# Kernel optimization log

Measured on AMD Instinct MI355X. Metric: run time of the kernel, lower is better.

The kernel has to match this reference:

```python
import jax, jax.numpy as jnp
import numpy as np

L_LAYERS, D, H, FF_MUL = 4, 512, 8, 4
VOCAB, SEQ, MEM, CMEM, RATIO = 32000, 1024, 1024, 256, 4
DH = D // H


def _ln(x, g, b):
    mu = jnp.mean(x, -1, keepdims=True)
    var = jnp.mean((x - mu) ** 2, -1, keepdims=True)
    return (x - mu) / jnp.sqrt(var + 1e-5) * g + b


def _heads(x):
    b, n, _ = x.shape
    return x.reshape(b, n, H, -1).transpose(0, 2, 1, 3)  # [b,h,n,dh]


def _shift(x):
    # relative-position shift trick, x: [b,h,i,j] -> [b,h,i,j]
    b, h, i, j = x.shape
    x = jnp.concatenate([x, jnp.zeros((b, h, i, i), x.dtype)], -1)
    l = i + j - 1
    x = x.reshape(b, h, i * (i + j))
    pad = (-x.shape[-1]) % l
    x = jnp.pad(x, ((0, 0), (0, 0), (0, pad))).reshape(b, h, -1, l)
    return x[:, :, :i, i - 1:]


def _conv(x, w, b):
    # x: [B,L,D], w: [D_out, D_in, RATIO] (OIH), stride=RATIO
    y = jax.lax.conv_general_dilated(x.transpose(0, 2, 1), w, (RATIO,), 'VALID',
                                     dimension_numbers=('NCH', 'OIH', 'NCH'))
    return y.transpose(0, 2, 1) + b


def _full_attn(q, k, v):
    dots = jnp.einsum('bhid,bhjd->bhij', q, k) * (q.shape[-1] ** -0.5)
    return jnp.einsum('bhij,bhjd->bhid', jax.nn.softmax(dots, -1), v)


def setup_inputs() -> dict:
    key = jax.random.key(0)
    ks = jax.random.split(key, 24)
    s = 0.02
    return {
        'seq': jax.random.randint(ks[0], (4, SEQ), 0, VOCAB),
        'mask': jnp.ones((4, SEQ), dtype=bool),
        'mems': jax.random.normal(ks[1], (L_LAYERS, 4, MEM, D)) * s,
        'cmems': jax.random.normal(ks[2], (L_LAYERS, 4, CMEM, D)) * s,
        'pos_emb': jax.random.normal(ks[3], (H, CMEM + MEM + SEQ, DH)) * s,
        'embed': jax.random.normal(ks[4], (VOCAB, D)) * s,
        'ln1_g': jnp.ones((L_LAYERS, D)), 'ln1_b': jnp.zeros((L_LAYERS, D)),
        'Wq': jax.random.normal(ks[5], (L_LAYERS, D, D)) * s,
        'Wkv': jax.random.normal(ks[6], (L_LAYERS, D, 2 * D)) * s,
        'Wo': jax.random.normal(ks[7], (L_LAYERS, D, D)) * s,
        'bo': jnp.zeros((L_LAYERS, D)),
        'conv_w': jax.random.normal(ks[8], (L_LAYERS, D, D, RATIO)) * s,
        'conv_b': jnp.zeros((L_LAYERS, D)),
        'ln2_g': jnp.ones((L_LAYERS, D)), 'ln2_b': jnp.zeros((L_LAYERS, D)),
        'W1': jax.random.normal(ks[9], (L_LAYERS, D, FF_MUL * D)) * s,
        'b1': jnp.zeros((L_LAYERS, FF_MUL * D)),
        'W2': jax.random.normal(ks[10], (L_LAYERS, FF_MUL * D, D)) * s,
        'b2': jnp.zeros((L_LAYERS, D)),
    }


def _forward(seq, mask, mems, cmems, pos_emb, embed, ln1_g, ln1_b, Wq, Wkv, Wo, bo,
             conv_w, conv_b, ln2_g, ln2_b, W1, b1, W2, b2):
    scale = DH ** -0.5
    x = embed[seq]  # [b,t,d]
    maskb = mask.astype(bool)
    new_mems, new_cmems = [], []
    aux_total = jnp.zeros((), x.dtype)
    w_acc = 0.0
    for l in range(L_LAYERS):
        mem, cmem = mems[l], cmems[l]
        xn = _ln(x, ln1_g[l], ln1_b[l])
        q = _heads(xn @ Wq[l])
        kv_in = jnp.concatenate([cmem, mem, xn], 1)  # [b,kv_len,d]
        kv_len = kv_in.shape[1]
        k, v = jnp.split(kv_in @ Wkv[l], 2, -1)
        k, v = _heads(k), _heads(v)
        dots = jnp.einsum('bhid,bhjd->bhij', q, k) * scale
        pe = pos_emb[:, -kv_len:]
        dots = dots + _shift(jnp.einsum('bhid,hjd->bhij', q, pe) * scale)
        m2 = maskb[:, None, :, None] & maskb[:, None, None, :]  # [b,1,t,t]
        m2 = jnp.pad(m2, ((0, 0), (0, 0), (0, 0), (kv_len - SEQ, 0)), constant_values=True)
        dots = jnp.where(m2, dots, -jnp.finfo(dots.dtype).max)
        attn = jax.nn.softmax(dots, -1)
        w_acc = w_acc + jnp.mean(jax.lax.stop_gradient(attn), axis=(0, 1))
        out = jnp.einsum('bhij,bhjd->bhid', attn, v)
        out = out.transpose(0, 2, 1, 3).reshape(x.shape[0], SEQ, D)
        x = x + out @ Wo[l] + bo[l]
        # FIFO memory update (queue normed x, evict oldest)
        queue = jnp.concatenate([mem, xn], 1)
        old_mem, new_mem = queue[:, :-MEM], queue[:, -MEM:]
        pad_amt = old_mem.shape[1] % RATIO
        if pad_amt:
            old_mem = jnp.pad(old_mem, ((0, 0), (pad_amt, 0), (0, 0)))
        comp = _conv(old_mem, conv_w[l], conv_b[l])
        new_cmem = jnp.concatenate([cmem, comp], 1)[:, -CMEM:]
        new_mems.append(new_mem)
        new_cmems.append(new_cmem)
        # reconstruction (attention-reconstruction) aux loss
        old_mem_d = jax.lax.stop_gradient(old_mem)
        comp2 = _conv(old_mem_d, conv_w[l], conv_b[l])
        ck, cv = jnp.split(comp2 @ jax.lax.stop_gradient(Wkv[l]), 2, -1)
        ck, cv = _heads(ck), _heads(cv)
        start = kv_len - min(mem.shape[1], MEM) - SEQ
        ok = jax.lax.stop_gradient(k[:, :, start:kv_len - SEQ])
        ov = jax.lax.stop_gradient(v[:, :, start:kv_len - SEQ])
        qd = jax.lax.stop_gradient(q)
        aux_total = aux_total + jnp.mean((_full_attn(qd, ok, ov) - _full_attn(qd, ck, cv)) ** 2)
        # feed-forward block (PreNorm + Residual), exact GELU like torch nn.GELU
        xn2 = _ln(x, ln2_g[l], ln2_b[l])
        x = x + jax.nn.gelu(xn2 @ W1[l] + b1[l], approximate=False) @ W2[l] + b2[l]
    return (x, jnp.stack(new_mems), jnp.stack(new_cmems),
            aux_total / L_LAYERS, w_acc / L_LAYERS)


def reference(seq, mask, mems, cmems, pos_emb, embed, ln1_g, ln1_b, Wq, Wkv, Wo, bo,
              conv_w, conv_b, ln2_g, ln2_b, W1, b1, W2, b2):
    return _forward(seq, mask, mems, cmems, pos_emb, embed, ln1_g, ln1_b, Wq, Wkv, Wo, bo,
                    conv_w, conv_b, ln2_g, ln2_b, W1, b1, W2, b2)
```

## Files before the change

### kernel.cpp

```cpp
#include <hip/hip_runtime.h>
#include <hip/hip_bf16.h>


typedef __hip_bfloat16 bf16;
typedef short s16x8 __attribute__((ext_vector_type(8)));
typedef float f32x4 __attribute__((ext_vector_type(4)));

__device__ __forceinline__ f32x4 mfma16(s16x8 a, s16x8 b, f32x4 c) {
  return __builtin_amdgcn_mfma_f32_16x16x32_bf16(a, b, c, 0, 0, 0);
}

typedef __attribute__((address_space(1))) const void gvoid;
typedef __attribute__((address_space(3))) void lvoid;
__device__ __forceinline__ void gll16(const void* g, void* l) {
  __builtin_amdgcn_global_load_lds((gvoid*)g, (lvoid*)l, 16, 0, 0);
}

__device__ __forceinline__ float b2f(unsigned short u) {
  return __uint_as_float(((unsigned)u) << 16);
}
__device__ __forceinline__ unsigned short f2bb(float f) {
  bf16 h = __float2bfloat16(f);
  return *reinterpret_cast<unsigned short*>(&h);
}
__device__ __forceinline__ float ldf(const float* p) { return *p; }
__device__ __forceinline__ float ldf(const bf16* p) { return __bfloat162float(*p); }
__device__ __forceinline__ float4 ld4(const float* p) { return *(const float4*)p; }
__device__ __forceinline__ float4 ld4(const bf16* p) {
  const ushort4 u = *(const ushort4*)p;
  return make_float4(b2f(u.x), b2f(u.y), b2f(u.z), b2f(u.w));
}
__device__ __forceinline__ void st4(float* p, float4 r) { *(float4*)p = r; }
__device__ __forceinline__ void st4(bf16* p, float4 r) {
  *(ushort4*)p = make_ushort4(f2bb(r.x), f2bb(r.y), f2bb(r.z), f2bb(r.w));
}
__device__ __forceinline__ void stf(float* p, float v) { *p = v; }
__device__ __forceinline__ void stf(bf16* p, float v) { *p = __float2bfloat16(v); }

__global__ void probe_k(const void* ln1g, unsigned* flag) {
  if (threadIdx.x == 0) {
    const unsigned short u = *(const unsigned short*)ln1g;
    *flag = (u == 0x3F80u) ? 1u : 0u;
  }
}

template <int BM, int AMODE, bool ADD, bool BIAS, bool GELU, typename TC>
__global__ __launch_bounds__(256) void mgemm_k(
    const bf16* __restrict__ A, const int lda, const bf16* __restrict__ Bt,
    TC* __restrict__ C, const int ldc, const float* __restrict__ bias,
    const int K) {
  constexpr int NF = (BM == 128) ? 4 : 2;
  __shared__ bf16 As[BM * 64];
  __shared__ bf16 Bs[128 * 64];
  const int t = threadIdx.x, w = t >> 6, lane = t & 63;
  const int g = lane >> 4, li = lane & 15;
  const int m0 = blockIdx.y * BM, n0 = blockIdx.x << 7;
  const int wrow = (BM == 128) ? ((w >> 1) << 6) : 0;
  const int wcol = (BM == 128) ? ((w & 1) << 6) : (w << 5);
  f32x4 acc[4][NF];
#pragma unroll
  for (int mf = 0; mf < 4; mf++)
#pragma unroll
    for (int nf = 0; nf < NF; nf++)
#pragma unroll
      for (int e = 0; e < 4; e++) acc[mf][nf][e] = 0.f;
  constexpr int ACH = BM / 32;
  const int srow = lane >> 3, s8 = lane & 7;
  for (int k0 = 0; k0 < K; k0 += 64) {
    __syncthreads();
#pragma unroll
    for (int it = 0; it < ACH; it++) {
      const int chunk = w * ACH + it;
      const int row = (chunk << 3) + srow;
      const int k8 = s8 ^ (row & 7);
      const bf16* src;
      if constexpr (AMODE == 0) {
        src = A + (size_t)(m0 + row) * lda + k0 + (k8 << 3);
      } else if constexpr (AMODE == 1) {
        const int m = m0 + row;
        src = A + ((size_t)((m >> 8) * 2304 + 256) << 9) + (m & 255) * 2048 +
              k0 + (k8 << 3);
      } else {
        const int m = m0 + row;
        src = A + ((size_t)((m >> 10) * 2304 + 1280 + (m & 1023)) << 9) + k0 +
              (k8 << 3);
      }
      gll16(src, As + (chunk << 9));
    }
#pragma unroll
    for (int it = 0; it < 4; it++) {
      const int chunk = (w << 2) + it;
      const int row = (chunk << 3) + srow;
      const int k8 = s8 ^ (row & 7);
      gll16(Bt + (size_t)(n0 + row) * K + k0 + (k8 << 3), Bs + (chunk << 9));
    }
    __syncthreads();
#pragma unroll
    for (int ks = 0; ks < 2; ks++) {
      s16x8 af[4];
#pragma unroll
      for (int mf = 0; mf < 4; mf++) {
        const int row = wrow + (mf << 4) + li;
        af[mf] = *reinterpret_cast<const s16x8*>(
            As + (row << 6) + ((((ks << 2) + g) ^ (row & 7)) << 3));
      }
#pragma unroll
      for (int nf = 0; nf < NF; nf++) {
        const int col = wcol + (nf << 4) + li;
        const s16x8 bfr = *reinterpret_cast<const s16x8*>(
            Bs + (col << 6) + ((((ks << 2) + g) ^ (col & 7)) << 3));
#pragma unroll
        for (int mf = 0; mf < 4; mf++)
          acc[mf][nf] = mfma16(af[mf], bfr, acc[mf][nf]);
      }
    }
  }
#pragma unroll
  for (int mf = 0; mf < 4; mf++)
#pragma unroll
    for (int nf = 0; nf < NF; nf++) {
      const int n = n0 + wcol + (nf << 4) + li;
      const float bv = BIAS ? bias[n] : 0.f;
#pragma unroll
      for (int r = 0; r < 4; r++) {
        const int m = m0 + wrow + (mf << 4) + (g << 2) + r;
        float v = acc[mf][nf][r] + bv;
        if constexpr (GELU) v = 0.5f * v * (1.0f + erff(v * 0.70710678118f));
        TC* cp = C + (size_t)m * ldc + n;
        if constexpr (ADD)
          *cp += v;
        else
          stf(cp, v);
      }
    }
}

template <bool REL, bool DIFF, typename TO>
__global__ __launch_bounds__(256) void flash_k(
    const bf16* __restrict__ q, const bf16* __restrict__ kbase,
    const bf16* __restrict__ vbase, const int kvlen, const int ldkv,
    const int bstride, const bf16* __restrict__ pe, float2* __restrict__ ml,
    TO* __restrict__ outp, const float* __restrict__ prior,
    float* __restrict__ auxsum) {
  __shared__ short k_s[4096];
  __shared__ short v_s[4096];
  __shared__ short p_s[4096];
  __shared__ short pe_s[REL ? 8192 : 8];
  __shared__ float t_s[REL ? 5376 : 4];
  __shared__ float red_s[4];
  const int t = threadIdx.x, w = t >> 6, lane = t & 63;
  const int g = lane >> 4, li = lane & 15;
  const int i0 = blockIdx.x << 6, h = blockIdx.y, b = blockIdx.z;
  const bf16* qp =
      q + (size_t)(b * 1024 + i0 + (w << 4) + li) * 512 + (h << 6) + (g << 3);
  const s16x8 qf0 = *reinterpret_cast<const s16x8*>(qp);
  const s16x8 qf1 = *reinterpret_cast<const s16x8*>(qp + 32);
  const bf16* kpb = kbase + (size_t)b * bstride + (h << 6);
  const bf16* vpb = vbase + (size_t)b * bstride + (h << 6);
  const bf16* peh = REL ? pe + (size_t)h * 147456 : nullptr;
  float mreg[4] = {-1e30f, -1e30f, -1e30f, -1e30f};
  float lreg[4] = {0.f, 0.f, 0.f, 0.f};
  f32x4 o[4];
#pragma unroll
  for (int nt = 0; nt < 4; nt++)
#pragma unroll
    for (int e = 0; e < 4; e++) o[nt][e] = 0.f;

  for (int j0 = 0; j0 < kvlen; j0 += 64) {
    const int ub0 = j0 - i0 + 960;
    const bool doT = REL && (ub0 < 2304);
    __syncthreads();
    {
      const int r2 = t >> 3, c8 = t & 7;
#pragma unroll
      for (int it = 0; it < 2; it++) {
        const int row = (it << 5) + r2;
        const size_t gof = (size_t)(j0 + row) * ldkv + (c8 << 3);
        const s16x8 kk = *reinterpret_cast<const s16x8*>(kpb + gof);
        *reinterpret_cast<s16x8*>(
            k_s + (((row << 6) + (c8 << 3)) ^ ((row & 7) << 3))) = kk;
        const s16x8 vv = *reinterpret_cast<const s16x8*>(vpb + gof);
#pragma unroll
        for (int e = 0; e < 8; e++) {
          const int d = (c8 << 3) + e;
          v_s[((d << 6) + row) ^ (((c8 ^ e) & 7) << 3)] = vv[e];
        }
      }
      if (doT) {
#pragma unroll
        for (int it = 0; it < 4; it++) {
          const int idx = (it << 8) + t;
          const int row = idx >> 3, pc8 = idx & 7;
          const int u = ub0 + row;
          s16x8 pv = {0, 0, 0, 0, 0, 0, 0, 0};
          if (u < 2304)
            pv = *reinterpret_cast<const s16x8*>(peh + ((size_t)u << 6) + (pc8 << 3));
          *reinterpret_cast<s16x8*>(
              pe_s + (((row << 6) + (pc8 << 3)) ^ ((row & 7) << 3))) = pv;
        }
      }
    }
    __syncthreads();
    f32x4 s[4];
#pragma unroll
    for (int nt = 0; nt < 4; nt++) {
#pragma unroll
      for (int e = 0; e < 4; e++) s[nt][e] = 0.f;
      const int rb = (((nt << 4) + li) << 6) + (g << 3);
      const int sw = (li & 7) << 3;
      const s16x8 kb0 = *reinterpret_cast<const s16x8*>(k_s + (rb ^ sw));
      const s16x8 kb1 = *reinterpret_cast<const s16x8*>(k_s + ((rb + 32) ^ sw));
      s[nt] = mfma16(qf0, kb0, s[nt]);
      s[nt] = mfma16(qf1, kb1, s[nt]);
    }
    if (doT) {
      float* tw = t_s + w * 1344;
      const int urb = 48 - (w << 4);
#pragma unroll
      for (int ut = 0; ut < 5; ut++) {
        f32x4 tt;
#pragma unroll
        for (int e = 0; e < 4; e++) tt[e] = 0.f;
        const int prb = ((urb + (ut << 4) + li) << 6) + (g << 3);
        const int sw = (li & 7) << 3;
        const s16x8 pb0 = *reinterpret_cast<const s16x8*>(pe_s + (prb ^ sw));
        const s16x8 pb1 = *reinterpret_cast<const s16x8*>(pe_s + ((prb + 32) ^ sw));
        tt = mfma16(qf0, pb0, tt);
        tt = mfma16(qf1, pb1, tt);
#pragma unroll
        for (int r = 0; r < 4; r++) tw[((g << 2) + r) * 84 + (ut << 4) + li] = tt[r];
      }
#pragma unroll
      for (int nt = 0; nt < 4; nt++)
#pragma unroll
        for (int r = 0; r < 4; r++)
          s[nt][r] += tw[((g << 2) + r) * 83 + (nt << 4) + li + 15];
    }
#pragma unroll
    for (int nt = 0; nt < 4; nt++)
#pragma unroll
      for (int e = 0; e < 4; e++) s[nt][e] *= 0.125f;
    float pr[4][4];
#pragma unroll
    for (int r = 0; r < 4; r++) {
      float tm = fmaxf(fmaxf(s[0][r], s[1][r]), fmaxf(s[2][r], s[3][r]));
#pragma unroll
      for (int off = 1; off < 16; off <<= 1) tm = fmaxf(tm, __shfl_xor(tm, off));
      const float mn = fmaxf(mreg[r], tm);
      const float al = __expf(mreg[r] - mn);
      mreg[r] = mn;
      float te = 0.f;
#pragma unroll
      for (int nt = 0; nt < 4; nt++) {
        pr[nt][r] = __expf(s[nt][r] - mn);
        te += pr[nt][r];
      }
#pragma unroll
      for (int off = 1; off < 16; off <<= 1) te += __shfl_xor(te, off);
      lreg[r] = lreg[r] * al + te;
#pragma unroll
      for (int nt = 0; nt < 4; nt++) o[nt][r] *= al;
    }
    short* pw = p_s + (w << 10);
#pragma unroll
    for (int nt = 0; nt < 4; nt++)
#pragma unroll
      for (int r = 0; r < 4; r++) {
        const int il = (g << 2) + r;
        pw[((il << 6) + (nt << 4) + li) ^ ((il & 7) << 3)] = (short)f2bb(pr[nt][r]);
      }
#pragma unroll
    for (int ks = 0; ks < 2; ks++) {
      const s16x8 pa = *reinterpret_cast<const s16x8*>(
          pw + (((li << 6) + (ks << 5) + (g << 3)) ^ ((li & 7) << 3)));
#pragma unroll
      for (int nt = 0; nt < 4; nt++) {
        const int d = (nt << 4) + li;
        const s16x8 vb = *reinterpret_cast<const s16x8*>(
            v_s + (((d << 6) + (ks << 5) + (g << 3)) ^ ((((d >> 3) ^ (d & 7)) & 7) << 3)));
        o[nt] = mfma16(pa, vb, o[nt]);
      }
    }
  }
  float rl[4];
#pragma unroll
  for (int r = 0; r < 4; r++) rl[r] = 1.0f / lreg[r];
  if constexpr (REL) {
    if (li == 0) {
#pragma unroll
      for (int r = 0; r < 4; r++)
        ml[(size_t)((b << 3) + h) * 1024 + i0 + (w << 4) + (g << 2) + r] =
            make_float2(mreg[r], lreg[r]);
    }
  }
  if constexpr (!DIFF) {
#pragma unroll
    for (int nt = 0; nt < 4; nt++)
#pragma unroll
      for (int r = 0; r < 4; r++) {
        const size_t adr = (size_t)(b * 1024 + i0 + (w << 4) + (g << 2) + r) * 512 +
                           (h << 6) + (nt << 4) + li;
        stf(outp + adr, o[nt][r] * rl[r]);
      }
  } else {
    float sq = 0.f;
#pragma unroll
    for (int nt = 0; nt < 4; nt++)
#pragma unroll
      for (int r = 0; r < 4; r++) {
        const size_t adr = (size_t)(b * 1024 + i0 + (w << 4) + (g << 2) + r) * 512 +
                           (h << 6) + (nt << 4) + li;
        const float dv = o[nt][r] * rl[r] - prior[adr];
        sq = fmaf(dv, dv, sq);
      }
#pragma unroll
    for (int off = 1; off < 64; off <<= 1) sq += __shfl_xor(sq, off);
    if (lane == 0) red_s[w] = sq;
    __syncthreads();
    if (t == 0) atomicAdd(auxsum, red_s[0] + red_s[1] + red_s[2] + red_s[3]);
  }
}

__global__ __launch_bounds__(256) void wacc_k(const bf16* __restrict__ q,
                                              const bf16* __restrict__ kv,
                                              const bf16* __restrict__ pe,
                                              const float2* __restrict__ ml,
                                              float* __restrict__ w_acc) {
  __shared__ short k_s[4096];
  __shared__ short pe_s[8192];
  __shared__ float t_s[5376];
  __shared__ float2 ml_s[64];
  const int t = threadIdx.x, w = t >> 6, lane = t & 63;
  const int g = lane >> 4, li = lane & 15;
  const int i0 = blockIdx.x << 6, j0 = blockIdx.y << 6;
  const int ub0 = j0 - i0 + 960;
  const bool doT = (ub0 < 2304);
  f32x4 acc[4];
#pragma unroll
  for (int nt = 0; nt < 4; nt++)
#pragma unroll
    for (int e = 0; e < 4; e++) acc[nt][e] = 0.f;
  for (int h = 0; h < 8; h++) {
    __syncthreads();
    if (doT) {
      const bf16* peh = pe + (size_t)h * 147456;
#pragma unroll
      for (int it = 0; it < 4; it++) {
        const int idx = (it << 8) + t;
        const int row = idx >> 3, pc8 = idx & 7;
        const int u = ub0 + row;
        s16x8 pv = {0, 0, 0, 0, 0, 0, 0, 0};
        if (u < 2304)
          pv = *reinterpret_cast<const s16x8*>(peh + ((size_t)u << 6) + (pc8 << 3));
        *reinterpret_cast<s16x8*>(
            pe_s + (((row << 6) + (pc8 << 3)) ^ ((row & 7) << 3))) = pv;
      }
    }
    for (int b = 0; b < 4; b++) {
      __syncthreads();
      {
        const int r2 = t >> 3, c8 = t & 7;
        const bf16* kpb = kv + (size_t)b * 2359296 + (h << 6);
#pragma unroll
        for (int it = 0; it < 2; it++) {
          const int row = (it << 5) + r2;
          const s16x8 kk = *reinterpret_cast<const s16x8*>(
              kpb + (size_t)(j0 + row) * 1024 + (c8 << 3));
          *reinterpret_cast<s16x8*>(
              k_s + (((row << 6) + (c8 << 3)) ^ ((row & 7) << 3))) = kk;
        }
        if (t < 64) {
          float2 v = ml[(size_t)((b << 3) + h) * 1024 + i0 + t];
          v.y = 1.0f / v.y;
          ml_s[t] = v;
        }
      }
      __syncthreads();
      const bf16* qp =
          q + (size_t)(b * 1024 + i0 + (w << 4) + li) * 512 + (h << 6) + (g << 3);
      const s16x8 qf0 = *reinterpret_cast<const s16x8*>(qp);
      const s16x8 qf1 = *reinterpret_cast<const s16x8*>(qp + 32);
      f32x4 s[4];
#pragma unroll
      for (int nt = 0; nt < 4; nt++) {
#pragma unroll
        for (int e = 0; e < 4; e++) s[nt][e] = 0.f;
        const int rb = (((nt << 4) + li) << 6) + (g << 3);
        const int sw = (li & 7) << 3;
        const s16x8 kb0 = *reinterpret_cast<const s16x8*>(k_s + (rb ^ sw));
        const s16x8 kb1 = *reinterpret_cast<const s16x8*>(k_s + ((rb + 32) ^ sw));
        s[nt] = mfma16(qf0, kb0, s[nt]);
        s[nt] = mfma16(qf1, kb1, s[nt]);
      }
      if (doT) {
        float* tw = t_s + w * 1344;
        const int urb = 48 - (w << 4);
#pragma unroll
        for (int ut = 0; ut < 5; ut++) {
          f32x4 tt;
#pragma unroll
          for (int e = 0; e < 4; e++) tt[e] = 0.f;
          const int prb = ((urb + (ut << 4) + li) << 6) + (g << 3);
          const int sw = (li & 7) << 3;
          const s16x8 pb0 = *reinterpret_cast<const s16x8*>(pe_s + (prb ^ sw));
          const s16x8 pb1 = *reinterpret_cast<const s16x8*>(pe_s + ((prb + 32) ^ sw));
          tt = mfma16(qf0, pb0, tt);
          tt = mfma16(qf1, pb1, tt);
#pragma unroll
          for (int r = 0; r < 4; r++)
            tw[((g << 2) + r) * 84 + (ut << 4) + li] = tt[r];
        }
#pragma unroll
        for (int nt = 0; nt < 4; nt++)
#pragma unroll
          for (int r = 0; r < 4; r++)
            s[nt][r] += tw[((g << 2) + r) * 83 + (nt << 4) + li + 15];
      }
#pragma unroll
      for (int nt = 0; nt < 4; nt++)
#pragma unroll
        for (int r = 0; r < 4; r++) {
          const float sv = s[nt][r] * 0.125f;
          const float2 st = ml_s[(w << 4) + (g << 2) + r];
          acc[nt][r] += __expf(sv - st.x) * st.y;
        }
    }
  }
#pragma unroll
  for (int nt = 0; nt < 4; nt++)
#pragma unroll
    for (int r = 0; r < 4; r++) {
      float* wp = w_acc + (size_t)(i0 + (w << 4) + (g << 2) + r) * 2304 + j0 +
                  (nt << 4) + li;
      *wp += acc[nt][r];
    }
}

template <typename TIN>
__global__ __launch_bounds__(256) void wtr_k(
    const TIN* __restrict__ Wq, const TIN* __restrict__ Wkv,
    const TIN* __restrict__ Wo, const TIN* __restrict__ W1,
    const TIN* __restrict__ W2, bf16* __restrict__ WT,
    const unsigned* flag, unsigned want) {
  if (*flag != want) return;
  __shared__ bf16 tile[64][65];
  int bx = blockIdx.x;
  const TIN* W;
  bf16* dst;
  int N, K;
  if (bx < 64) {
    W = Wq; dst = WT; N = 512; K = 512;
  } else if (bx < 192) {
    W = Wkv; dst = WT + 262144; N = 1024; K = 512; bx -= 64;
  } else if (bx < 256) {
    W = Wo; dst = WT + 786432; N = 512; K = 512; bx -= 192;
  } else if (bx < 512) {
    W = W1; dst = WT + 1048576; N = 2048; K = 512; bx -= 256;
  } else {
    W = W2; dst = WT + 2097152; N = 512; K = 2048; bx -= 512;
  }
  const int tn = N >> 6;
  const int kt = bx / tn, nt = bx - kt * tn;
  const int k0 = kt << 6, n0 = nt << 6;
  const int t = threadIdx.x;
#pragma unroll
  for (int i = 0; i < 16; i++) {
    const int idx = (i << 8) + t;
    const int kr = idx >> 6, nc = idx & 63;
    tile[kr][nc] = __float2bfloat16(ldf(W + (size_t)(k0 + kr) * N + n0 + nc));
  }
  __syncthreads();
#pragma unroll
  for (int i = 0; i < 16; i++) {
    const int idx = (i << 8) + t;
    const int nr = idx >> 6, kc = idx & 63;
    dst[(size_t)(n0 + nr) * K + k0 + kc] = tile[kc][nr];
  }
}

template <typename TIN>
__global__ void wcp_k(const TIN* __restrict__ cw, bf16* __restrict__ WcT,
                      const unsigned* flag, unsigned want) {
  if (*flag != want) return;
  const int id = blockIdx.x * 256 + threadIdx.x;
  const int o = id >> 11, p = id & 2047;
  const int r = p >> 9, i = p & 511;
  WcT[id] = __float2bfloat16(ldf(cw + ((size_t)o << 11) + (i << 2) + r));
}

template <typename TIN>
__global__ void kvb_k(const TIN* __restrict__ cmem, const TIN* __restrict__ mem,
                      bf16* __restrict__ kvin, const unsigned* flag, unsigned want) {
  if (*flag != want) return;
  const int id = blockIdx.x * 256 + threadIdx.x;
  const int row = id >> 7, c4 = (id & 127) << 2;
  const int b = row / 1280, j = row - b * 1280;
  const TIN* src = (j < 256) ? cmem + (((size_t)(b * 256 + j)) << 9) + c4
                             : mem + (((size_t)(b * 1024 + j - 256)) << 9) + c4;
  st4(kvin + (((size_t)(b * 2304 + j)) << 9) + c4, ld4(src));
}

template <typename TIN>
__global__ void bcvt_k(const TIN* __restrict__ bo, const TIN* __restrict__ cb,
                       const TIN* __restrict__ b1, const TIN* __restrict__ b2,
                       float* __restrict__ bws, const unsigned* flag, unsigned want) {
  if (*flag != want) return;
  const int id = blockIdx.x * 256 + threadIdx.x;
  const int l = id / 3584, r = id - l * 3584;
  float v;
  if (r < 512) v = ldf(bo + l * 512 + r);
  else if (r < 1024) v = ldf(cb + l * 512 + r - 512);
  else if (r < 3072) v = ldf(b1 + l * 2048 + r - 1024);
  else v = ldf(b2 + l * 512 + r - 3072);
  bws[id] = v;
}

template <typename TIN, typename TY>
__global__ __launch_bounds__(256) void ln_k(const float* __restrict__ x,
                                            const TIN* __restrict__ g,
                                            const TIN* __restrict__ bta,
                                            TY* __restrict__ y, bf16* kvx,
                                            const unsigned* flag, unsigned want) {
  if (*flag != want) return;
  const int w = threadIdx.x >> 6, lane = threadIdx.x & 63;
  const size_t row = (size_t)blockIdx.x * 4 + w;
  const float* xr = x + row * 512;
  float v[8], s = 0, ss = 0;
#pragma unroll
  for (int i = 0; i < 8; i++) {
    v[i] = xr[lane + (i << 6)];
    s += v[i];
    ss = fmaf(v[i], v[i], ss);
  }
#pragma unroll
  for (int off = 1; off < 64; off <<= 1) {
    s += __shfl_xor(s, off);
    ss += __shfl_xor(ss, off);
  }
  const float mu = s * (1.0f / 512.0f);
  const float var = ss * (1.0f / 512.0f) - mu * mu;
  const float inv = rsqrtf(var + 1e-5f);
  bf16* k2 = kvx ? kvx + (((row >> 10) * 2304 + 1280 + (row & 1023)) << 9) : nullptr;
#pragma unroll
  for (int i = 0; i < 8; i++) {
    const int c = lane + (i << 6);
    const float val = (v[i] - mu) * inv * ldf(g + c) + ldf(bta + c);
    stf(y + row * 512 + c, val);
    if (k2) k2[c] = __float2bfloat16(val);
  }
}

template <typename TIN>
__global__ void embed_k(const int* __restrict__ seq, const TIN* __restrict__ emb,
                        float* __restrict__ x, const unsigned* flag, unsigned want) {
  if (*flag != want) return;
  const int row = blockIdx.x;
  const int tok = seq[row];
  const TIN* e = emb + (size_t)tok * 512;
  float* xr = x + (size_t)row * 512;
  for (int c = threadIdx.x; c < 512; c += 256) xr[c] = ldf(e + c);
}

template <typename TIN>
__global__ void cvtpe_k(const TIN* __restrict__ pe, bf16* __restrict__ peb,
                        const unsigned* flag, unsigned want) {
  if (*flag != want) return;
  const int i = blockIdx.x * 256 + threadIdx.x;
  peb[i] = __float2bfloat16(ldf(pe + i));
}

__global__ void zero_k(float* __restrict__ p, int n) {
  for (int i = blockIdx.x * 256 + threadIdx.x; i < n; i += gridDim.x * 256) p[i] = 0.0f;
}

template <typename TOUT>
__global__ void cpy_k(const bf16* __restrict__ s, TOUT* __restrict__ d, int n,
                      const unsigned* flag, unsigned want) {
  if (*flag != want) return;
  for (int i = blockIdx.x * 256 + threadIdx.x; i < n; i += gridDim.x * 256)
    stf(d + i, ldf(s + i));
}

template <typename TOUT>
__global__ void f2bs_k(const float* __restrict__ s, TOUT* __restrict__ d, float sc,
                       int n, const unsigned* flag, unsigned want) {
  if (*flag != want) return;
  for (int i = blockIdx.x * 256 + threadIdx.x; i < n; i += gridDim.x * 256)
    stf(d + i, s[i] * sc);
}

template <typename TOUT>
__global__ void fin_aux_k(const float* __restrict__ acc, TOUT* __restrict__ d,
                          const unsigned* flag, unsigned want) {
  if (*flag != want) return;
  if (threadIdx.x == 0) stf(d, acc[0] * (1.0f / 8388608.0f));
}

extern "C" void kernel_launch(void* const* d_in, const int* in_sizes, int n_in,
                              void* d_out, int out_size, void* d_ws, size_t ws_size,
                              hipStream_t stream) {
  typedef const bf16 CB;
  typedef const float CF;
  const int* seq = (const int*)d_in[0];
  CB *mems_b = (CB*)d_in[2], *cmems_b = (CB*)d_in[3], *pe_b = (CB*)d_in[4],
     *emb_b = (CB*)d_in[5], *l1g_b = (CB*)d_in[6], *l1b_b = (CB*)d_in[7],
     *Wq_b = (CB*)d_in[8], *Wkv_b = (CB*)d_in[9], *Wo_b = (CB*)d_in[10],
     *bo_b = (CB*)d_in[11], *cw_b = (CB*)d_in[12], *cb_b = (CB*)d_in[13],
     *l2g_b = (CB*)d_in[14], *l2b_b = (CB*)d_in[15], *W1_b = (CB*)d_in[16],
     *b1_b = (CB*)d_in[17], *W2_b = (CB*)d_in[18], *b2_b = (CB*)d_in[19];
  CF *mems_f = (CF*)d_in[2], *cmems_f = (CF*)d_in[3], *pe_f = (CF*)d_in[4],
     *emb_f = (CF*)d_in[5], *l1g_f = (CF*)d_in[6], *l1b_f = (CF*)d_in[7],
     *Wq_f = (CF*)d_in[8], *Wkv_f = (CF*)d_in[9], *Wo_f = (CF*)d_in[10],
     *bo_f = (CF*)d_in[11], *cw_f = (CF*)d_in[12], *cb_f = (CF*)d_in[13],
     *l2g_f = (CF*)d_in[14], *l2b_f = (CF*)d_in[15], *W1_f = (CF*)d_in[16],
     *b1_f = (CF*)d_in[17], *W2_f = (CF*)d_in[18], *b2_f = (CF*)d_in[19];
  bf16* outb = (bf16*)d_out;
  float* outf = (float*)d_out;

  float* ws = (float*)d_ws;
  float* x = ws;
  bf16* q = (bf16*)(ws + 2097152);
  bf16* kv = (bf16*)(ws + 3145728);
  bf16* mid = (bf16*)(ws + 3145728);
  float* region = ws + 7864320;
  bf16* attn_o = (bf16*)region;
  float* aux1 = region;
  bf16* xn2 = (bf16*)region;
  bf16* ckcv = (bf16*)(ws + 9961472);
  float* w_acc = ws + 10485760;
  bf16* cmp_ws = (bf16*)(ws + 12845056);
  float2* ml = (float2*)(ws + 13369344);
  float* auxsum = ws + 13434880;
  unsigned* flag = (unsigned*)(ws + 13434881);
  bf16* pe_w = (bf16*)(ws + 13434884);
  float* bias_ws = ws + 14024708;
  bf16* kvin = (bf16*)(ws + 14039044);
  bf16* WT = (bf16*)(ws + 16398340);

  probe_k<<<1, 64, 0, stream>>>(d_in[6], flag);
  zero_k<<<2048, 256, 0, stream>>>(w_acc, 2359296);
  zero_k<<<1, 256, 0, stream>>>(auxsum, 1);
  embed_k<bf16><<<4096, 256, 0, stream>>>(seq, emb_b, x, flag, 1);
  embed_k<float><<<4096, 256, 0, stream>>>(seq, emb_f, x, flag, 0);
  cvtpe_k<bf16><<<4608, 256, 0, stream>>>(pe_b, pe_w, flag, 1);
  cvtpe_k<float><<<4608, 256, 0, stream>>>(pe_f, pe_w, flag, 0);
  bcvt_k<bf16><<<56, 256, 0, stream>>>(bo_b, cb_b, b1_b, b2_b, bias_ws, flag, 1);
  bcvt_k<float><<<56, 256, 0, stream>>>(bo_f, cb_f, b1_f, b2_f, bias_ws, flag, 0);

  for (int l = 0; l < 4; l++) {
    bf16* xnl_b = outb + 2097152 + (size_t)l * 2097152;
    float* xnl_f = outf + 2097152 + (size_t)l * 2097152;
    bf16* cmp_b = outb + 10485760 + (size_t)l * 524288;
    float* cmp_f = outf + 10485760 + (size_t)l * 524288;
    const float* bl = bias_ws + l * 3584;

    wtr_k<bf16><<<768, 256, 0, stream>>>(Wq_b + (size_t)l * 262144,
        Wkv_b + (size_t)l * 524288, Wo_b + (size_t)l * 262144,
        W1_b + (size_t)l * 1048576, W2_b + (size_t)l * 1048576, WT, flag, 1);
    wtr_k<float><<<768, 256, 0, stream>>>(Wq_f + (size_t)l * 262144,
        Wkv_f + (size_t)l * 524288, Wo_f + (size_t)l * 262144,
        W1_f + (size_t)l * 1048576, W2_f + (size_t)l * 1048576, WT, flag, 0);
    wcp_k<bf16><<<4096, 256, 0, stream>>>(cw_b + (size_t)l * 1048576, WT + 3145728, flag, 1);
    wcp_k<float><<<4096, 256, 0, stream>>>(cw_f + (size_t)l * 1048576, WT + 3145728, flag, 0);
    kvb_k<bf16><<<2560, 256, 0, stream>>>(cmems_b + (size_t)l * 524288,
                                          mems_b + (size_t)l * 2097152, kvin, flag, 1);
    kvb_k<float><<<2560, 256, 0, stream>>>(cmems_f + (size_t)l * 524288,
                                           mems_f + (size_t)l * 2097152, kvin, flag, 0);
    ln_k<bf16, bf16><<<1024, 256, 0, stream>>>(x, l1g_b + l * 512, l1b_b + l * 512,
                                               xnl_b, kvin, flag, 1);
    ln_k<float, float><<<1024, 256, 0, stream>>>(x, l1g_f + l * 512, l1b_f + l * 512,
                                                 xnl_f, kvin, flag, 0);
    mgemm_k<64, 2, false, false, false, bf16><<<dim3(4, 64), 256, 0, stream>>>(
        kvin, 512, WT, q, 512, nullptr, 512);
    mgemm_k<128, 0, false, false, false, bf16><<<dim3(8, 72), 256, 0, stream>>>(
        kvin, 512, WT + 262144, kv, 1024, nullptr, 512);
    flash_k<true, false, bf16><<<dim3(16, 8, 4), 256, 0, stream>>>(
        q, kv, kv + 512, 2304, 1024, 2359296, pe_w, ml, attn_o, nullptr, nullptr);
    wacc_k<<<dim3(16, 36), 256, 0, stream>>>(q, kv, pe_w, ml, w_acc);
    mgemm_k<64, 0, true, true, false, float><<<dim3(4, 64), 256, 0, stream>>>(
        attn_o, 512, WT + 786432, x, 512, bl, 512);
    mgemm_k<64, 1, false, true, false, bf16><<<dim3(4, 16), 256, 0, stream>>>(
        kvin, 0, WT + 3145728, cmp_ws, 512, bl + 512, 2048);
    cpy_k<bf16><<<512, 256, 0, stream>>>(cmp_ws, cmp_b, 524288, flag, 1);
    cpy_k<float><<<512, 256, 0, stream>>>(cmp_ws, cmp_f, 524288, flag, 0);
    mgemm_k<64, 0, false, false, false, bf16><<<dim3(8, 16), 256, 0, stream>>>(
        cmp_ws, 512, WT + 262144, ckcv, 1024, nullptr, 512);
    flash_k<false, false, float><<<dim3(16, 8, 4), 256, 0, stream>>>(
        q, kv + 262144, kv + 262144 + 512, 1024, 1024, 2359296, nullptr, nullptr,
        aux1, nullptr, nullptr);
    flash_k<false, true, float><<<dim3(16, 8, 4), 256, 0, stream>>>(
        q, ckcv, ckcv + 512, 256, 1024, 262144, nullptr, nullptr,
        (float*)nullptr, aux1, auxsum);
    ln_k<bf16, bf16><<<1024, 256, 0, stream>>>(x, l2g_b + l * 512, l2b_b + l * 512,
                                               xn2, nullptr, flag, 1);
    ln_k<float, bf16><<<1024, 256, 0, stream>>>(x, l2g_f + l * 512, l2b_f + l * 512,
                                                xn2, nullptr, flag, 0);
    mgemm_k<128, 0, false, true, true, bf16><<<dim3(16, 32), 256, 0, stream>>>(
        xn2, 512, WT + 1048576, mid, 2048, bl + 1024, 512);
    mgemm_k<64, 0, true, true, false, float><<<dim3(4, 64), 256, 0, stream>>>(
        mid, 2048, WT + 2097152, x, 512, bl + 3072, 2048);
  }

  f2bs_k<bf16><<<2048, 256, 0, stream>>>(x, outb, 1.0f, 2097152, flag, 1);
  f2bs_k<float><<<2048, 256, 0, stream>>>(x, outf, 1.0f, 2097152, flag, 0);
  f2bs_k<bf16><<<2048, 256, 0, stream>>>(w_acc, outb + 12582913, 1.0f / 128.0f, 2359296, flag, 1);
  f2bs_k<float><<<2048, 256, 0, stream>>>(w_acc, outf + 12582913, 1.0f / 128.0f, 2359296, flag, 0);
  fin_aux_k<bf16><<<1, 64, 0, stream>>>(auxsum, outb + 12582912, flag, 1);
  fin_aux_k<float><<<1, 64, 0, stream>>>(auxsum, outf + 12582912, flag, 0);
}
```

Measured before the change: 2.031 ms.

## Double-buffer K/V staging in flash and wacc kernels, drop LDS pos-emb tiles

The flash and wacc attention kernels now double-buffer K tiles in LDS, staged with asynchronous global_load_lds, and prefetch the next V tile into registers, so loads overlap compute and each iteration needs one barrier instead of two. The relative-position term is computed from pos-emb fragments loaded straight into registers and shifted with cross-lane shuffles rather than LDS staging plus a float scratch buffer, which cuts LDS use and raises possible occupancy. Out-of-range pos-emb rows read from a new zero row buffer. The flash grid is flattened so the 8 heads of one query tile are adjacent, aux1 moves to its own workspace region, and wacc loops over head and batch with prefetching, at the cost of more register pressure.

```diff
diff --git a/kernel.cpp b/kernel.cpp
--- a/kernel.cpp
+++ b/kernel.cpp
@@ -139,18 +139,20 @@
 __global__ __launch_bounds__(256) void flash_k(
     const bf16* __restrict__ q, const bf16* __restrict__ kbase,
     const bf16* __restrict__ vbase, const int kvlen, const int ldkv,
-    const int bstride, const bf16* __restrict__ pe, float2* __restrict__ ml,
+    const int bstride, const bf16* __restrict__ pe,
+    const bf16* __restrict__ zrow, float2* __restrict__ ml,
     TO* __restrict__ outp, const float* __restrict__ prior,
     float* __restrict__ auxsum) {
-  __shared__ short k_s[4096];
-  __shared__ short v_s[4096];
+  __shared__ short k_s[2][4096];
+  __shared__ short v_s[2][4096];
   __shared__ short p_s[4096];
-  __shared__ short pe_s[REL ? 8192 : 8];
-  __shared__ float t_s[REL ? 5376 : 4];
-  __shared__ float red_s[4];
   const int t = threadIdx.x, w = t >> 6, lane = t & 63;
   const int g = lane >> 4, li = lane & 15;
-  const int i0 = blockIdx.x << 6, h = blockIdx.y, b = blockIdx.z;
+  const int bid = blockIdx.x;
+  const int h = bid & 7;
+  const int sl = bid >> 3;
+  const int b = sl >> 4;
+  const int i0 = (sl & 15) << 6;
   const bf16* qp =
       q + (size_t)(b * 1024 + i0 + (w << 4) + li) * 512 + (h << 6) + (g << 3);
   const s16x8 qf0 = *reinterpret_cast<const s16x8*>(qp);
@@ -158,6 +160,8 @@
   const bf16* kpb = kbase + (size_t)b * bstride + (h << 6);
   const bf16* vpb = vbase + (size_t)b * bstride + (h << 6);
   const bf16* peh = REL ? pe + (size_t)h * 147456 : nullptr;
+  const int vr = t >> 3, vc8 = t & 7;
+  const int kr = lane >> 3, kc8 = lane & 7;
   float mreg[4] = {-1e30f, -1e30f, -1e30f, -1e30f};
   float lreg[4] = {0.f, 0.f, 0.f, 0.f};
   f32x4 o[4];
@@ -166,75 +170,94 @@
 #pragma unroll
     for (int e = 0; e < 4; e++) o[nt][e] = 0.f;
 
+#define STAGE_K(J0, BUF)                                                      \
+  {                                                                           \
+    _Pragma("unroll") for (int it = 0; it < 2; it++) {                        \
+      const int chunk = (w << 1) + it;                                        \
+      const int row = (chunk << 3) + kr;                                      \
+      gll16(kpb + (size_t)((J0) + row) * ldkv + ((kc8 ^ (row & 7)) << 3),     \
+            &k_s[BUF][chunk << 9]);                                           \
+    }                                                                         \
+  }
+#define LOAD_V(J0, VA, VB)                                                    \
+  {                                                                           \
+    VA = *reinterpret_cast<const s16x8*>(                                     \
+        vpb + (size_t)((J0) + vr) * ldkv + (vc8 << 3));                       \
+    VB = *reinterpret_cast<const s16x8*>(                                     \
+        vpb + (size_t)((J0) + 32 + vr) * ldkv + (vc8 << 3));                  \
+  }
+#define WRITE_V(BUF, VA, VB)                                                  \
+  {                                                                           \
+    _Pragma("unroll") for (int e = 0; e < 8; e++) {                           \
+      const int d = (vc8 << 3) + e;                                           \
+      const int sw = ((vc8 ^ e) & 7) << 3;                                    \
+      v_s[BUF][((d << 6) + vr) ^ sw] = VA[e];                                 \
+      v_s[BUF][((d << 6) + (vr + 32)) ^ sw] = VB[e];                          \
+    }                                                                         \
+  }
+
+  {
+    s16x8 va, vb2;
+    STAGE_K(0, 0);
+    LOAD_V(0, va, vb2);
+    WRITE_V(0, va, vb2);
+    __syncthreads();
+  }
+  int cur = 0;
   for (int j0 = 0; j0 < kvlen; j0 += 64) {
+    const bool last = (j0 + 64 >= kvlen);
+    s16x8 nva, nvb;
+    if (!last) {
+      LOAD_V(j0 + 64, nva, nvb);
+      STAGE_K(j0 + 64, cur ^ 1);
+    }
     const int ub0 = j0 - i0 + 960;
     const bool doT = REL && (ub0 < 2304);
-    __syncthreads();
-    {
-      const int r2 = t >> 3, c8 = t & 7;
-#pragma unroll
-      for (int it = 0; it < 2; it++) {
-        const int row = (it << 5) + r2;
-        const size_t gof = (size_t)(j0 + row) * ldkv + (c8 << 3);
-        const s16x8 kk = *reinterpret_cast<const s16x8*>(kpb + gof);
-        *reinterpret_cast<s16x8*>(
-            k_s + (((row << 6) + (c8 << 3)) ^ ((row & 7) << 3))) = kk;
-        const s16x8 vv = *reinterpret_cast<const s16x8*>(vpb + gof);
-#pragma unroll
-        for (int e = 0; e < 8; e++) {
-          const int d = (c8 << 3) + e;
-          v_s[((d << 6) + row) ^ (((c8 ^ e) & 7) << 3)] = vv[e];
-        }
-      }
-      if (doT) {
-#pragma unroll
-        for (int it = 0; it < 4; it++) {
-          const int idx = (it << 8) + t;
-          const int row = idx >> 3, pc8 = idx & 7;
-          const int u = ub0 + row;
-          s16x8 pv = {0, 0, 0, 0, 0, 0, 0, 0};
-          if (u < 2304)
-            pv = *reinterpret_cast<const s16x8*>(peh + ((size_t)u << 6) + (pc8 << 3));
-          *reinterpret_cast<s16x8*>(
-              pe_s + (((row << 6) + (pc8 << 3)) ^ ((row & 7) << 3))) = pv;
-        }
-      }
-    }
-    __syncthreads();
+    s16x8 pb[5][2];
+    if (REL && doT) {
+      const int ubase = j0 - i0 + 1008 - (w << 4);
+#pragma unroll
+      for (int ut = 0; ut < 5; ut++) {
+        const int u = ubase + (ut << 4) + li;
+        const bf16* pp = (u < 2304) ? peh + ((size_t)u << 6) : zrow;
+        pb[ut][0] = *reinterpret_cast<const s16x8*>(pp + (g << 3));
+        pb[ut][1] = *reinterpret_cast<const s16x8*>(pp + 32 + (g << 3));
+      }
+    }
     f32x4 s[4];
 #pragma unroll
     for (int nt = 0; nt < 4; nt++) {
 #pragma unroll
       for (int e = 0; e < 4; e++) s[nt][e] = 0.f;
-      const int rb = (((nt << 4) + li) << 6) + (g << 3);
-      const int sw = (li & 7) << 3;
-      const s16x8 kb0 = *reinterpret_cast<const s16x8*>(k_s + (rb ^ sw));
-      const s16x8 kb1 = *reinterpret_cast<const s16x8*>(k_s + ((rb + 32) ^ sw));
+      const int j = (nt << 4) + li;
+      const s16x8 kb0 = *reinterpret_cast<const s16x8*>(
+          &k_s[cur][(j << 6) + ((g ^ (j & 7)) << 3)]);
+      const s16x8 kb1 = *reinterpret_cast<const s16x8*>(
+          &k_s[cur][(j << 6) + (((g + 4) ^ (j & 7)) << 3)]);
       s[nt] = mfma16(qf0, kb0, s[nt]);
       s[nt] = mfma16(qf1, kb1, s[nt]);
     }
-    if (doT) {
-      float* tw = t_s + w * 1344;
-      const int urb = 48 - (w << 4);
+    if (REL && doT) {
+      f32x4 t5[5];
 #pragma unroll
       for (int ut = 0; ut < 5; ut++) {
-        f32x4 tt;
-#pragma unroll
-        for (int e = 0; e < 4; e++) tt[e] = 0.f;
-        const int prb = ((urb + (ut << 4) + li) << 6) + (g << 3);
-        const int sw = (li & 7) << 3;
-        const s16x8 pb0 = *reinterpret_cast<const s16x8*>(pe_s + (prb ^ sw));
-        const s16x8 pb1 = *reinterpret_cast<const s16x8*>(pe_s + ((prb + 32) ^ sw));
-        tt = mfma16(qf0, pb0, tt);
-        tt = mfma16(qf1, pb1, tt);
-#pragma unroll
-        for (int r = 0; r < 4; r++) tw[((g << 2) + r) * 84 + (ut << 4) + li] = tt[r];
-      }
-#pragma unroll
-      for (int nt = 0; nt < 4; nt++)
-#pragma unroll
-        for (int r = 0; r < 4; r++)
-          s[nt][r] += tw[((g << 2) + r) * 83 + (nt << 4) + li + 15];
+#pragma unroll
+        for (int e = 0; e < 4; e++) t5[ut][e] = 0.f;
+        t5[ut] = mfma16(qf0, pb[ut][0], t5[ut]);
+        t5[ut] = mfma16(qf1, pb[ut][1], t5[ut]);
+      }
+#pragma unroll
+      for (int r = 0; r < 4; r++) {
+        const int il = (g << 2) + r;
+        const int local = li - il + 15;
+        const int srcl = (g << 4) | (local & 15);
+        float tv[5];
+#pragma unroll
+        for (int ut = 0; ut < 5; ut++) tv[ut] = __shfl(t5[ut][r], srcl);
+        const bool hi = local >= 16;
+#pragma unroll
+        for (int nt = 0; nt < 4; nt++) s[nt][r] += hi ? tv[nt + 1] : tv[nt];
+      }
     }
 #pragma unroll
     for (int nt = 0; nt < 4; nt++)
@@ -277,11 +300,18 @@
       for (int nt = 0; nt < 4; nt++) {
         const int d = (nt << 4) + li;
         const s16x8 vb = *reinterpret_cast<const s16x8*>(
-            v_s + (((d << 6) + (ks << 5) + (g << 3)) ^ ((((d >> 3) ^ (d & 7)) & 7) << 3)));
+            &v_s[cur][((d << 6) + (ks << 5) + (g << 3)) ^
+                      ((((d >> 3) ^ (d & 7)) & 7) << 3)]);
         o[nt] = mfma16(pa, vb, o[nt]);
       }
     }
-  }
+    if (!last) WRITE_V(cur ^ 1, nva, nvb);
+    __syncthreads();
+    cur ^= 1;
+  }
+#undef STAGE_K
+#undef LOAD_V
+#undef WRITE_V
   float rl[4];
 #pragma unroll
   for (int r = 0; r < 4; r++) rl[r] = 1.0f / lreg[r];
@@ -315,117 +345,113 @@
       }
 #pragma unroll
     for (int off = 1; off < 64; off <<= 1) sq += __shfl_xor(sq, off);
-    if (lane == 0) red_s[w] = sq;
+    float* fl = reinterpret_cast<float*>(p_s);
+    if (lane == 0) fl[w] = sq;
     __syncthreads();
-    if (t == 0) atomicAdd(auxsum, red_s[0] + red_s[1] + red_s[2] + red_s[3]);
+    if (t == 0) atomicAdd(auxsum, fl[0] + fl[1] + fl[2] + fl[3]);
   }
 }
 
 __global__ __launch_bounds__(256) void wacc_k(const bf16* __restrict__ q,
                                               const bf16* __restrict__ kv,
                                               const bf16* __restrict__ pe,
+                                              const bf16* __restrict__ zrow,
                                               const float2* __restrict__ ml,
                                               float* __restrict__ w_acc) {
-  __shared__ short k_s[4096];
-  __shared__ short pe_s[8192];
-  __shared__ float t_s[5376];
-  __shared__ float2 ml_s[64];
+  __shared__ short k_s[2][4096];
   const int t = threadIdx.x, w = t >> 6, lane = t & 63;
   const int g = lane >> 4, li = lane & 15;
   const int i0 = blockIdx.x << 6, j0 = blockIdx.y << 6;
   const int ub0 = j0 - i0 + 960;
   const bool doT = (ub0 < 2304);
+  const int kr = lane >> 3, kc8 = lane & 7;
   f32x4 acc[4];
 #pragma unroll
   for (int nt = 0; nt < 4; nt++)
 #pragma unroll
     for (int e = 0; e < 4; e++) acc[nt][e] = 0.f;
-  for (int h = 0; h < 8; h++) {
-    __syncthreads();
+
+#define STAGE_KW(HB, BUF)                                                     \
+  {                                                                           \
+    const int hh = (HB) >> 2, bb = (HB)&3;                                    \
+    const bf16* kpb = kv + (size_t)bb * 2359296 + (hh << 6);                  \
+    _Pragma("unroll") for (int it = 0; it < 2; it++) {                        \
+      const int chunk = (w << 1) + it;                                        \
+      const int row = (chunk << 3) + kr;                                      \
+      gll16(kpb + (size_t)(j0 + row) * 1024 + ((kc8 ^ (row & 7)) << 3),       \
+            &k_s[BUF][chunk << 9]);                                           \
+    }                                                                         \
+  }
+  STAGE_KW(0, 0);
+  __syncthreads();
+  int cur = 0;
+  for (int hb = 0; hb < 32; hb++) {
+    const int h = hb >> 2, b = hb & 3;
+    if (hb < 31) STAGE_KW(hb + 1, cur ^ 1);
+    const bf16* qp =
+        q + (size_t)(b * 1024 + i0 + (w << 4) + li) * 512 + (h << 6) + (g << 3);
+    const s16x8 qf0 = *reinterpret_cast<const s16x8*>(qp);
+    const s16x8 qf1 = *reinterpret_cast<const s16x8*>(qp + 32);
+    s16x8 pb[5][2];
     if (doT) {
       const bf16* peh = pe + (size_t)h * 147456;
-#pragma unroll
-      for (int it = 0; it < 4; it++) {
-        const int idx = (it << 8) + t;
-        const int row = idx >> 3, pc8 = idx & 7;
-        const int u = ub0 + row;
-        s16x8 pv = {0, 0, 0, 0, 0, 0, 0, 0};
-        if (u < 2304)
-          pv = *reinterpret_cast<const s16x8*>(peh + ((size_t)u << 6) + (pc8 << 3));
-        *reinterpret_cast<s16x8*>(
-            pe_s + (((row << 6) + (pc8 << 3)) ^ ((row & 7) << 3))) = pv;
-      }
-    }
-    for (int b = 0; b < 4; b++) {
-      __syncthreads();
-      {
-        const int r2 = t >> 3, c8 = t & 7;
-        const bf16* kpb = kv + (size_t)b * 2359296 + (h << 6);
-#pragma unroll
-        for (int it = 0; it < 2; it++) {
-          const int row = (it << 5) + r2;
-          const s16x8 kk = *reinterpret_cast<const s16x8*>(
-              kpb + (size_t)(j0 + row) * 1024 + (c8 << 3));
-          *reinterpret_cast<s16x8*>(
-              k_s + (((row << 6) + (c8 << 3)) ^ ((row & 7) << 3))) = kk;
-        }
-        if (t < 64) {
-          float2 v = ml[(size_t)((b << 3) + h) * 1024 + i0 + t];
-          v.y = 1.0f / v.y;
-          ml_s[t] = v;
-        }
-      }
-      __syncthreads();
-      const bf16* qp =
-          q + (size_t)(b * 1024 + i0 + (w << 4) + li) * 512 + (h << 6) + (g << 3);
-      const s16x8 qf0 = *reinterpret_cast<const s16x8*>(qp);
-      const s16x8 qf1 = *reinterpret_cast<const s16x8*>(qp + 32);
-      f32x4 s[4];
-#pragma unroll
-      for (int nt = 0; nt < 4; nt++) {
-#pragma unroll
-        for (int e = 0; e < 4; e++) s[nt][e] = 0.f;
-        const int rb = (((nt << 4) + li) << 6) + (g << 3);
-        const int sw = (li & 7) << 3;
-        const s16x8 kb0 = *reinterpret_cast<const s16x8*>(k_s + (rb ^ sw));
-        const s16x8 kb1 = *reinterpret_cast<const s16x8*>(k_s + ((rb + 32) ^ sw));
-        s[nt] = mfma16(qf0, kb0, s[nt]);
-        s[nt] = mfma16(qf1, kb1, s[nt]);
-      }
-      if (doT) {
-        float* tw = t_s + w * 1344;
-        const int urb = 48 - (w << 4);
-#pragma unroll
-        for (int ut = 0; ut < 5; ut++) {
-          f32x4 tt;
-#pragma unroll
-          for (int e = 0; e < 4; e++) tt[e] = 0.f;
-          const int prb = ((urb + (ut << 4) + li) << 6) + (g << 3);
-          const int sw = (li & 7) << 3;
-          const s16x8 pb0 = *reinterpret_cast<const s16x8*>(pe_s + (prb ^ sw));
-          const s16x8 pb1 = *reinterpret_cast<const s16x8*>(pe_s + ((prb + 32) ^ sw));
-          tt = mfma16(qf0, pb0, tt);
-          tt = mfma16(qf1, pb1, tt);
-#pragma unroll
-          for (int r = 0; r < 4; r++)
-            tw[((g << 2) + r) * 84 + (ut << 4) + li] = tt[r];
-        }
-#pragma unroll
-        for (int nt = 0; nt < 4; nt++)
-#pragma unroll
-          for (int r = 0; r < 4; r++)
-            s[nt][r] += tw[((g << 2) + r) * 83 + (nt << 4) + li + 15];
-      }
+      const int ubase = j0 - i0 + 1008 - (w << 4);
+#pragma unroll
+      for (int ut = 0; ut < 5; ut++) {
+        const int u = ubase + (ut << 4) + li;
+        const bf16* pp = (u < 2304) ? peh + ((size_t)u << 6) : zrow;
+        pb[ut][0] = *reinterpret_cast<const s16x8*>(pp + (g << 3));
+        pb[ut][1] = *reinterpret_cast<const s16x8*>(pp + 32 + (g << 3));
+      }
+    }
+    f32x4 s[4];
+#pragma unroll
+    for (int nt = 0; nt < 4; nt++) {
+#pragma unroll
+      for (int e = 0; e < 4; e++) s[nt][e] = 0.f;
+      const int j = (nt << 4) + li;
+      const s16x8 kb0 = *reinterpret_cast<const s16x8*>(
+          &k_s[cur][(j << 6) + ((g ^ (j & 7)) << 3)]);
+      const s16x8 kb1 = *reinterpret_cast<const s16x8*>(
+          &k_s[cur][(j << 6) + (((g + 4) ^ (j & 7)) << 3)]);
+      s[nt] = mfma16(qf0, kb0, s[nt]);
+      s[nt] = mfma16(qf1, kb1, s[nt]);
+    }
+    if (doT) {
+      f32x4 t5[5];
+#pragma unroll
+      for (int ut = 0; ut < 5; ut++) {
+#pragma unroll
+        for (int e = 0; e < 4; e++) t5[ut][e] = 0.f;
+        t5[ut] = mfma16(qf0, pb[ut][0], t5[ut]);
+        t5[ut] = mfma16(qf1, pb[ut][1], t5[ut]);
+      }
+#pragma unroll
+      for (int r = 0; r < 4; r++) {
+        const int il = (g << 2) + r;
+        const int local = li - il + 15;
+        const int srcl = (g << 4) | (local & 15);
+        float tv[5];
+#pragma unroll
+        for (int ut = 0; ut < 5; ut++) tv[ut] = __shfl(t5[ut][r], srcl);
+        const bool hi = local >= 16;
+#pragma unroll
+        for (int nt = 0; nt < 4; nt++) s[nt][r] += hi ? tv[nt + 1] : tv[nt];
+      }
+    }
+#pragma unroll
+    for (int r = 0; r < 4; r++) {
+      const float2 st =
+          ml[(size_t)((b << 3) + h) * 1024 + i0 + (w << 4) + (g << 2) + r];
+      const float rr = 1.0f / st.y;
 #pragma unroll
       for (int nt = 0; nt < 4; nt++)
-#pragma unroll
-        for (int r = 0; r < 4; r++) {
-          const float sv = s[nt][r] * 0.125f;
-          const float2 st = ml_s[(w << 4) + (g << 2) + r];
-          acc[nt][r] += __expf(sv - st.x) * st.y;
-        }
-    }
-  }
+        acc[nt][r] += __expf(s[nt][r] * 0.125f - st.x) * rr;
+    }
+    __syncthreads();
+    cur ^= 1;
+  }
+#undef STAGE_KW
 #pragma unroll
   for (int nt = 0; nt < 4; nt++)
 #pragma unroll
@@ -624,7 +650,6 @@
   bf16* mid = (bf16*)(ws + 3145728);
   float* region = ws + 7864320;
   bf16* attn_o = (bf16*)region;
-  float* aux1 = region;
   bf16* xn2 = (bf16*)region;
   bf16* ckcv = (bf16*)(ws + 9961472);
   float* w_acc = ws + 10485760;
@@ -636,10 +661,14 @@
   float* bias_ws = ws + 14024708;
   bf16* kvin = (bf16*)(ws + 14039044);
   bf16* WT = (bf16*)(ws + 16398340);
+  float* aux1 = ws + 18757636;
+  float* zrow_f = ws + 20854788;
+  bf16* zrow = (bf16*)zrow_f;
 
   probe_k<<<1, 64, 0, stream>>>(d_in[6], flag);
   zero_k<<<2048, 256, 0, stream>>>(w_acc, 2359296);
   zero_k<<<1, 256, 0, stream>>>(auxsum, 1);
+  zero_k<<<1, 64, 0, stream>>>(zrow_f, 32);
   embed_k<bf16><<<4096, 256, 0, stream>>>(seq, emb_b, x, flag, 1);
   embed_k<float><<<4096, 256, 0, stream>>>(seq, emb_f, x, flag, 0);
   cvtpe_k<bf16><<<4608, 256, 0, stream>>>(pe_b, pe_w, flag, 1);
@@ -674,9 +703,10 @@
         kvin, 512, WT, q, 512, nullptr, 512);
     mgemm_k<128, 0, false, false, false, bf16><<<dim3(8, 72), 256, 0, stream>>>(
         kvin, 512, WT + 262144, kv, 1024, nullptr, 512);
-    flash_k<true, false, bf16><<<dim3(16, 8, 4), 256, 0, stream>>>(
-        q, kv, kv + 512, 2304, 1024, 2359296, pe_w, ml, attn_o, nullptr, nullptr);
-    wacc_k<<<dim3(16, 36), 256, 0, stream>>>(q, kv, pe_w, ml, w_acc);
+    flash_k<true, false, bf16><<<512, 256, 0, stream>>>(
+        q, kv, kv + 512, 2304, 1024, 2359296, pe_w, zrow, ml, attn_o,
+        nullptr, nullptr);
+    wacc_k<<<dim3(16, 36), 256, 0, stream>>>(q, kv, pe_w, zrow, ml, w_acc);
     mgemm_k<64, 0, true, true, false, float><<<dim3(4, 64), 256, 0, stream>>>(
         attn_o, 512, WT + 786432, x, 512, bl, 512);
     mgemm_k<64, 1, false, true, false, bf16><<<dim3(4, 16), 256, 0, stream>>>(
@@ -685,11 +715,11 @@
     cpy_k<float><<<512, 256, 0, stream>>>(cmp_ws, cmp_f, 524288, flag, 0);
     mgemm_k<64, 0, false, false, false, bf16><<<dim3(8, 16), 256, 0, stream>>>(
         cmp_ws, 512, WT + 262144, ckcv, 1024, nullptr, 512);
-    flash_k<false, false, float><<<dim3(16, 8, 4), 256, 0, stream>>>(
-        q, kv + 262144, kv + 262144 + 512, 1024, 1024, 2359296, nullptr, nullptr,
-        aux1, nullptr, nullptr);
-    flash_k<false, true, float><<<dim3(16, 8, 4), 256, 0, stream>>>(
-        q, ckcv, ckcv + 512, 256, 1024, 262144, nullptr, nullptr,
+    flash_k<false, false, float><<<512, 256, 0, stream>>>(
+        q, kv + 262144, kv + 262144 + 512, 1024, 1024, 2359296, nullptr, zrow,
+        nullptr, aux1, nullptr, nullptr);
+    flash_k<false, true, float><<<512, 256, 0, stream>>>(
+        q, ckcv, ckcv + 512, 256, 1024, 262144, nullptr, zrow, nullptr,
         (float*)nullptr, aux1, auxsum);
     ln_k<bf16, bf16><<<1024, 256, 0, stream>>>(x, l2g_b + l * 512, l2b_b + l * 512,
                                                xn2, nullptr, flag, 1);
```

Result: slower. 2.342 ms (+15.3%).
